# Optimization experiments

Measured on AMD Instinct MI355X. Metric: run time of the kernel, lower is better.

Reference implementation:

```python
import jax, jax.numpy as jnp
import numpy as np

EPS = 0.05
ITERS = 3


def setup_inputs() -> dict:
    key = jax.random.key(0)
    ks = jax.random.split(key, 20)
    B, C, H, W, TD = 2, 256, 64, 64, 512
    s = 0.02
    inp = {
        "img_feat": jax.random.normal(ks[0], (B, C, H, W), jnp.float32),
        "txt_feat": jax.random.normal(ks[1], (B, TD), jnp.float32),
        "density_map": jax.random.uniform(ks[2], (B, 1, H, W), jnp.float32),
        # text_proj
        "Wt": jax.random.normal(ks[3], (C, TD), jnp.float32) * s,
        "bt": jnp.zeros((C,), jnp.float32),
        # gamma_fc / beta_fc
        "Wg": jax.random.normal(ks[4], (C, C), jnp.float32) * s,
        "bg": jnp.zeros((C,), jnp.float32),
        "Wb": jax.random.normal(ks[5], (C, C), jnp.float32) * s,
        "bb": jnp.zeros((C,), jnp.float32),
        # out_proj 1x1 conv as [O, I]
        "Wo": jax.random.normal(ks[6], (C, C), jnp.float32) * s,
        "bo": jnp.zeros((C,), jnp.float32),
        # heatmap head: conv3x3 -> BN -> ReLU -> conv1x1
        "Wc1": jax.random.normal(ks[7], (C // 2, C, 3, 3), jnp.float32) * s,
        "bc1": jnp.zeros((C // 2,), jnp.float32),
        "bn_g": jnp.ones((C // 2,), jnp.float32),
        "bn_b": jnp.zeros((C // 2,), jnp.float32),
        "Wc2": jax.random.normal(ks[8], (2, C // 2), jnp.float32) * s,
        "bc2": jnp.zeros((2,), jnp.float32),
    }
    return inp


def reference(img_feat, txt_feat, density_map, Wt, bt, Wg, bg, Wb, bb,
              Wo, bo, Wc1, bc1, bn_g, bn_b, Wc2, bc2):
    B, C, H, W = img_feat.shape
    N = H * W

    # FiLM-style modulation from text
    txt_emb = txt_feat @ Wt.T + bt                         # [B, C]
    gamma = (txt_emb @ Wg.T + bg)[:, :, None, None]        # [B, C, 1, 1]
    beta = (txt_emb @ Wb.T + bb)[:, :, None, None]
    mod = img_feat * (1.0 + gamma) + beta                  # [B, C, H, W]

    source_feat = mod.reshape(B, C, N).transpose(0, 2, 1)  # [B, N, C]

    # marginals
    target = jax.nn.relu(density_map.reshape(B, N)) + 1e-6
    q = target / jnp.sum(target, axis=1, keepdims=True)    # [B, N]
    p = jnp.full((B, N), 1.0 / N, img_feat.dtype)

    # cosine-similarity cost and Gibbs kernel
    src_n = source_feat / jnp.maximum(
        jnp.linalg.norm(source_feat, axis=2, keepdims=True), 1e-12)
    sim = jnp.einsum('bnc,bmc->bnm', src_n, src_n)         # [B, N, N]
    K = jnp.exp(-(1.0 - sim) / EPS)

    # Sinkhorn iterations (fixed count)
    u = jnp.ones_like(p)
    v = jnp.ones_like(q)
    for _ in range(ITERS):
        v = q / (jnp.einsum('bnm,bn->bm', K, u) + 1e-8)
        u = p / (jnp.einsum('bnm,bm->bn', K, v) + 1e-8)

    T = u[:, :, None] * K * v[:, None, :]                  # transport plan
    fused = jnp.einsum('bnm,bnc->bmc', T, source_feat)     # T^T @ source
    fused = fused.transpose(0, 2, 1).reshape(B, C, H, W)

    out_feat = img_feat + jnp.einsum('oc,bchw->bohw', Wo, fused) + bo[None, :, None, None]

    # heatmap head
    h = jax.lax.conv_general_dilated(
        out_feat, Wc1, window_strides=(1, 1), padding='SAME',
        dimension_numbers=('NCHW', 'OIHW', 'NCHW')) + bc1[None, :, None, None]
    m = jnp.mean(h, axis=(0, 2, 3), keepdims=True)
    var = jnp.var(h, axis=(0, 2, 3), keepdims=True)
    h = (h - m) * jax.lax.rsqrt(var + 1e-5)
    h = jax.nn.relu(h * bn_g[None, :, None, None] + bn_b[None, :, None, None])
    heatmap = jnp.einsum('oc,bchw->bohw', Wc2, h) + bc2[None, :, None, None]

    return out_feat, heatmap
```

## Files before the change

### kernel.cpp

```cpp
#include <hip/hip_runtime.h>
#include <stdint.h>

#define B_   2
#define C_   256
#define N_   4096
#define TD_  512
#define OC_  128
#define PW_  66
#define PA_  4356

typedef float  f32x4  __attribute__((ext_vector_type(4)));
typedef short  bf16x8 __attribute__((ext_vector_type(8)));
typedef unsigned short u16;
typedef unsigned char  u8;

__device__ __forceinline__ u16 f2bf(float x){
  union { float f; uint32_t u; } v; v.f = x;
  uint32_t r = v.u + 0x7fffu + ((v.u >> 16) & 1u);
  return (u16)(r >> 16);
}
__device__ __forceinline__ uint32_t f2e5m2(float x){
  x = fminf(fmaxf(x, -57344.f), 57344.f);
  union { _Float16 h; u16 u; } c; c.h = (_Float16)x;
  uint32_t hb = c.u;
  return ((hb + 0x7fu + ((hb >> 8) & 1u)) >> 8) & 0xffu;
}
__device__ __forceinline__ float e5m2f(uint32_t byte){
  union { u16 u; _Float16 h; } c; c.u = (u16)(byte << 8);
  return (float)c.h;
}

__device__ __forceinline__ void gld_lds16(const void* g, void* l){
  __builtin_amdgcn_global_load_lds(
      (const __attribute__((address_space(1))) unsigned int*)g,
      (__attribute__((address_space(3))) unsigned int*)l,
      16, 0, 0);
}

__global__ __launch_bounds__(1024) void k_prep(
    const float* __restrict__ txt, const float* __restrict__ Wt, const float* __restrict__ bt,
    const float* __restrict__ Wg, const float* __restrict__ bg,
    const float* __restrict__ Wb, const float* __restrict__ bb,
    const float* __restrict__ dens, const float* __restrict__ Wo, const float* __restrict__ Wc1,
    float* __restrict__ gamma, float* __restrict__ beta,
    float* __restrict__ q, float* __restrict__ u,
    u16* __restrict__ Wo_bf, u16* __restrict__ Wc1r, u16* __restrict__ P){
  int bid = blockIdx.x;
  int t = threadIdx.x;
  if (bid < 2){
    int b = bid;
    __shared__ float ts[TD_];
    __shared__ float te[C_];
    if (t < TD_) ts[t] = txt[b*TD_ + t];
    __syncthreads();
    {
      int c = t >> 2, p = t & 3;
      const float4* w4 = (const float4*)(Wt + (size_t)c*TD_ + p*128);
      const float4* t4 = (const float4*)(ts + p*128);
      float a = 0.f;
      #pragma unroll 8
      for (int j = 0; j < 32; j++){
        float4 wv = w4[j], tv = t4[j];
        a += wv.x*tv.x + wv.y*tv.y + wv.z*tv.z + wv.w*tv.w;
      }
      a += __shfl_xor(a, 1);
      a += __shfl_xor(a, 2);
      if (p == 0) te[c] = a + bt[c];
    }
    __syncthreads();
    {
      int c = t >> 2, qb = (t >> 1) & 1, p = t & 1;
      const float* W = qb ? Wb : Wg;
      const float4* w4 = (const float4*)(W + (size_t)c*C_ + p*128);
      const float4* t4 = (const float4*)(te + p*128);
      float a = 0.f;
      #pragma unroll 8
      for (int j = 0; j < 32; j++){
        float4 wv = w4[j], tv = t4[j];
        a += wv.x*tv.x + wv.y*tv.y + wv.z*tv.z + wv.w*tv.w;
      }
      a += __shfl_xor(a, 1);
      if (p == 0){
        if (qb) beta[b*C_ + c]  = a + bb[c];
        else    gamma[b*C_ + c] = a + bg[c];
      }
    }
  } else if (bid < 4){
    int b = bid - 2;
    __shared__ float red[1024];
    float s = 0.f;
    for (int i = t; i < N_; i += 1024){ float v = fmaxf(dens[b*N_ + i], 0.f) + 1e-6f; s += v; }
    red[t] = s; __syncthreads();
    for (int o = 512; o; o >>= 1){ if (t < o) red[t] += red[t + o]; __syncthreads(); }
    float invs = 1.f / red[0];
    for (int i = t; i < N_; i += 1024){
      float v = fmaxf(dens[b*N_ + i], 0.f) + 1e-6f;
      q[b*N_ + i] = v*invs;
      u[b*N_ + i] = 1.f;
    }
  } else if (bid < 292){
    int i = (bid - 4)*1024 + t;
    if (i < C_*C_) Wo_bf[i] = f2bf(Wo[i]);
    if (i < 9*OC_*C_){
      int s = i / (OC_*C_); int rem = i - s*(OC_*C_);
      int oc = rem >> 8; int ic = rem & 255;
      Wc1r[i] = f2bf(Wc1[((size_t)(oc*C_ + ic))*9 + s]);
    }
  } else {
    int g = (bid - 292)*1024 + t;
    if (g < 16640){
      int px_i = g >> 5, seg = g & 31;
      int b = (px_i >= 260) ? 1 : 0;
      int i = px_i - b*260;
      int row, col;
      if (i < 66)      { row = 0;  col = i; }
      else if (i < 132){ row = 65; col = i - 66; }
      else { int i2 = i - 132; row = 1 + (i2 >> 1); col = (i2 & 1) ? 65 : 0; }
      uint4 z; z.x = 0; z.y = 0; z.z = 0; z.w = 0;
      *(uint4*)((char*)P + ((size_t)(b*PA_ + row*PW_ + col))*512 + seg*16) = z;
    }
  }
}

__global__ __launch_bounds__(256) void k_build(
    const float* __restrict__ img, const float* __restrict__ gamma, const float* __restrict__ beta,
    u16* __restrict__ Sn){
  int b = blockIdx.y; int n0 = blockIdx.x*64;
  __shared__ float tile[C_][65];
  __shared__ float pss[4][64];
  __shared__ float inv[64];
  int t = threadIdx.x;
  int x = t & 63, cb = t >> 6;
  float ss = 0.f;
  for (int k = 0; k < 64; k++){
    int c = cb*64 + k;
    float v = img[((size_t)(b*C_ + c))*N_ + n0 + x];
    v = v*(1.f + gamma[b*C_ + c]) + beta[b*C_ + c];
    tile[c][x] = v;
    ss += v*v;
  }
  pss[cb][x] = ss;
  __syncthreads();
  if (t < 64){
    float s = pss[0][t] + pss[1][t] + pss[2][t] + pss[3][t];
    float nrm = sqrtf(s);
    inv[t] = 1.f / fmaxf(nrm, 1e-12f);
  }
  __syncthreads();
  for (int i = 0; i < 64; i++){
    int idx = i*256 + t;
    int c = idx & 255, nl = idx >> 8;
    Sn[((size_t)(b*N_ + n0 + nl))*C_ + c] = f2bf(tile[c][nl]*inv[nl]);
  }
}

__global__ __launch_bounds__(256) void k_simK(const u16* __restrict__ Sn, u8* __restrict__ K8,
                                              u8* __restrict__ flags){
  int idx = blockIdx.x;
  int b = blockIdx.z;
  int nt = (int)((sqrtf(8.f*idx + 1.f) - 1.f)*0.5f);
  while ((nt+1)*(nt+2)/2 <= idx) nt++;
  while (nt*(nt+1)/2 > idx) nt--;
  int mt = idx - nt*(nt+1)/2;
  __shared__ char smem[32768];
  __shared__ int fred[4];
  int t = threadIdx.x; int w = t >> 6; int l = t & 63;
  int wm = w >> 1, wn = w & 1;
  f32x4 acc[4][4] = {};
  const char* Ab = (const char*)(Sn + ((size_t)(b*N_ + mt*128))*C_);
  const char* Bb = (const char*)(Sn + ((size_t)(b*N_ + nt*128))*C_);
  for (int step = 0; step < 4; step++){
    __syncthreads();
    for (int r = 0; r < 4; r++){
      int off = r*4096 + t*16;
      int row = off >> 7;
      int col = (off & 127) ^ ((row & 7) << 4);
      gld_lds16(Ab + (size_t)row*512 + step*128 + col, smem + off);
      gld_lds16(Bb + (size_t)row*512 + step*128 + col, smem + 16384 + off);
    }
    __syncthreads();
    for (int kk = 0; kk < 2; kk++){
      bf16x8 af[4], bfv[4];
      for (int i = 0; i < 4; i++){
        int ra = wm*64 + i*16 + (l & 15);
        af[i]  = *(const bf16x8*)(smem + ((ra*128 + kk*64 + (l>>4)*16) ^ ((ra & 7) << 4)));
        int rb = wn*64 + i*16 + (l & 15);
        bfv[i] = *(const bf16x8*)(smem + 16384 + ((rb*128 + kk*64 + (l>>4)*16) ^ ((rb & 7) << 4)));
      }
      for (int i = 0; i < 4; i++)
        for (int j = 0; j < 4; j++)
          acc[i][j] = __builtin_amdgcn_mfma_f32_16x16x32_bf16(af[i], bfv[j], acc[i][j], 0, 0, 0);
    }
  }
  float tmax = -1.f;
  for (int i = 0; i < 4; i++)
    for (int j = 0; j < 4; j++){
      f32x4 a = acc[i][j];
      tmax = fmaxf(tmax, fmaxf(fmaxf(a[0], a[1]), fmaxf(a[2], a[3])));
    }
  int nz = __any(tmax > 0.40f) ? 1 : 0;
  if (l == 0) fred[w] = nz;
  __syncthreads();
  int F = fred[0] | fred[1] | fred[2] | fred[3];
  if (t == 0){
    flags[b*1024 + nt*32 + mt] = (u8)F;
    if (mt != nt) flags[b*1024 + mt*32 + nt] = (u8)F;
  }
  size_t gb  = ((size_t)(b*N_ + nt*128))*N_ + mt*128;
  size_t gb2 = ((size_t)(b*N_ + mt*128))*N_ + nt*128;
  if (!F){
    uint4 z; z.x = 0; z.y = 0; z.z = 0; z.w = 0;
    for (int p = 0; p < 4; p++){
      int id2 = p*256 + t;
      int R = id2 >> 3, sl = id2 & 7;
      *(uint4*)(K8 + gb + (size_t)R*N_ + sl*16) = z;
      if (mt != nt) *(uint4*)(K8 + gb2 + (size_t)R*N_ + sl*16) = z;
    }
    return;
  }
  u8* tile = (u8*)smem;
  uint32_t wds[4][4];
  for (int i = 0; i < 4; i++)
    for (int j = 0; j < 4; j++){
      int R  = wn*64 + j*16 + (l & 15);
      int Cc = wm*64 + i*16 + ((l >> 4) << 2);
      uint32_t wd =  f2e5m2(__expf((acc[i][j][0] - 1.f)*20.f))
                  | (f2e5m2(__expf((acc[i][j][1] - 1.f)*20.f)) << 8)
                  | (f2e5m2(__expf((acc[i][j][2] - 1.f)*20.f)) << 16)
                  | (f2e5m2(__expf((acc[i][j][3] - 1.f)*20.f)) << 24);
      wds[i][j] = wd;
      *(uint32_t*)(tile + ((R*128 + Cc) ^ ((R & 7) << 4))) = wd;
    }
  __syncthreads();
  for (int p = 0; p < 4; p++){
    int id2 = p*256 + t;
    int R = id2 >> 3, sl = id2 & 7;
    uint4 vv = *(const uint4*)(tile + ((R*128 + sl*16) ^ ((R & 7) << 4)));
    *(uint4*)(K8 + gb + (size_t)R*N_ + sl*16) = vv;
  }
  if (mt != nt){
    __syncthreads();
    for (int i = 0; i < 4; i++)
      for (int j = 0; j < 4; j++){
        int m0 = wm*64 + i*16 + ((l >> 4) << 2);
        int n  = wn*64 + j*16 + (l & 15);
        uint32_t wd = wds[i][j];
        for (int r = 0; r < 4; r++){
          int R = m0 + r;
          tile[(R*128 + n) ^ ((R & 7) << 4)] = (u8)(wd >> (8*r));
        }
      }
    __syncthreads();
    for (int p = 0; p < 4; p++){
      int id2 = p*256 + t;
      int R = id2 >> 3, sl = id2 & 7;
      uint4 vv = *(const uint4*)(tile + ((R*128 + sl*16) ^ ((R & 7) << 4)));
      *(uint4*)(K8 + gb2 + (size_t)R*N_ + sl*16) = vv;
    }
  }
}

__global__ __launch_bounds__(256) void k_matvec(
    const u8* __restrict__ K8, const u8* __restrict__ flags, const float* __restrict__ x,
    const float* __restrict__ q, float* __restrict__ out, int use_q){
  int w = threadIdx.x >> 6, l = threadIdx.x & 63;
  int row = blockIdx.x*4 + w;
  int b = row >> 12;
  const u8* kp = K8 + (size_t)row*N_;
  const float* xp = x + (size_t)b*N_;
  const u8* fr = flags + b*1024 + ((row & 4095) >> 7)*32;
  float s = 0.f;
  for (int it = 0; it < 8; it++){
    uint32_t f4 = *(const uint32_t*)(fr + it*4);
    if (!f4) continue;
    int n0 = it*512 + l*8;
    uint2 kv = *(const uint2*)(kp + n0);
    float4 x0 = *(const float4*)(xp + n0);
    float4 x1 = *(const float4*)(xp + n0 + 4);
    s += e5m2f( kv.x        & 0xff)*x0.x + e5m2f((kv.x >>  8) & 0xff)*x0.y
       + e5m2f((kv.x >> 16) & 0xff)*x0.z + e5m2f( kv.x >> 24        )*x0.w;
    s += e5m2f( kv.y        & 0xff)*x1.x + e5m2f((kv.y >>  8) & 0xff)*x1.y
       + e5m2f((kv.y >> 16) & 0xff)*x1.z + e5m2f( kv.y >> 24        )*x1.w;
  }
  for (int o = 32; o; o >>= 1) s += __shfl_down(s, o);
  if (l == 0){
    float marg = use_q ? q[row] : 2.44140625e-4f;
    out[row] = marg / (s + 1e-8f);
  }
}

__global__ __launch_bounds__(256) void k_uS(
    const float* __restrict__ img, const float* __restrict__ gamma, const float* __restrict__ beta,
    const float* __restrict__ u, u8* __restrict__ uS8){
  size_t i = ((size_t)blockIdx.x*256 + threadIdx.x)*4;
  int n = (int)(i & (N_ - 1));
  size_t bc = i >> 12;
  int b = (int)(bc >> 8);
  float gm = 1.f + gamma[bc];
  float bt = beta[bc];
  float4 v  = *(const float4*)(img + i);
  float4 uu = *(const float4*)(u + (size_t)b*N_ + n);
  uint32_t o =  f2e5m2((v.x*gm + bt)*uu.x)
             | (f2e5m2((v.y*gm + bt)*uu.y) << 8)
             | (f2e5m2((v.z*gm + bt)*uu.z) << 16)
             | (f2e5m2((v.w*gm + bt)*uu.w) << 24);
  *(uint32_t*)(uS8 + i) = o;
}

__global__ __launch_bounds__(256) void k_fused_part(
    const u8* __restrict__ K8, const u8* __restrict__ uS8, const u8* __restrict__ flags,
    _Float16* __restrict__ part){
  int ct = blockIdx.x & 1, ks = blockIdx.x >> 1;
  int mt = blockIdx.y, b = blockIdx.z;
  __shared__ char smem[32768];
  int t = threadIdx.x, w = t >> 6, l = t & 63;
  int wc = w >> 1, wm = w & 1;
  f32x4 acc[4][4] = {};
  const u8* Ab = uS8 + ((size_t)(b*C_ + ct*128))*N_ + ks*1024;
  const u8* Bb = K8  + ((size_t)(b*N_ + mt*128))*N_ + ks*1024;
  const u8* fr = flags + b*1024 + mt*32 + ks*8;
  for (int step = 0; step < 8; step++){
    if (!fr[step]) continue;
    __syncthreads();
    for (int r = 0; r < 4; r++){
      int off = r*4096 + t*16;
      int row = off >> 7;
      int col = (off & 127) ^ ((row & 7) << 4);
      gld_lds16(Ab + (size_t)row*N_ + step*128 + col, smem + off);
      gld_lds16(Bb + (size_t)row*N_ + step*128 + col, smem + 16384 + off);
    }
    __syncthreads();
    for (int kk = 0; kk < 4; kk++){
      long av[4], bv[4];
      for (int i = 0; i < 4; i++){
        int ra = wc*64 + i*16 + (l & 15);
        av[i] = *(const long*)(smem + ((ra*128 + kk*32 + (l>>4)*8) ^ ((ra & 7) << 4)));
        int rb = wm*64 + i*16 + (l & 15);
        bv[i] = *(const long*)(smem + 16384 + ((rb*128 + kk*32 + (l>>4)*8) ^ ((rb & 7) << 4)));
      }
      for (int i = 0; i < 4; i++)
        for (int j = 0; j < 4; j++)
          acc[i][j] = __builtin_amdgcn_mfma_f32_16x16x32_bf8_bf8(av[i], bv[j], acc[i][j], 0, 0, 0);
    }
  }
  _Float16* pp = part + ((size_t)(ks*2 + b))*N_*C_;
  for (int i = 0; i < 4; i++)
    for (int j = 0; j < 4; j++){
      int c0 = ct*128 + wc*64 + i*16 + ((l >> 4) << 2);
      int m  = mt*128 + wm*64 + j*16 + (l & 15);
      union { _Float16 h[4]; ushort4 u; } pk;
      pk.h[0] = (_Float16)acc[i][j][0];
      pk.h[1] = (_Float16)acc[i][j][1];
      pk.h[2] = (_Float16)acc[i][j][2];
      pk.h[3] = (_Float16)acc[i][j][3];
      *(ushort4*)(pp + (size_t)m*C_ + c0) = pk.u;
    }
}

__global__ __launch_bounds__(256) void k_reduce(
    const _Float16* __restrict__ part, const float* __restrict__ vvec, u16* __restrict__ fused){
  int idx = blockIdx.x*256 + threadIdx.x;
  int c0 = (idx & 63) * 4;
  int bm = idx >> 6;
  float vm = vvec[bm];
  float s0 = 0.f, s1 = 0.f, s2 = 0.f, s3 = 0.f;
  int b = bm >> 12, m = bm & 4095;
  for (int sp = 0; sp < 4; sp++){
    union { ushort4 u; _Float16 h[4]; } pk;
    pk.u = *(const ushort4*)(part + (((size_t)(sp*2 + b))*N_ + m)*C_ + c0);
    s0 += (float)pk.h[0]; s1 += (float)pk.h[1];
    s2 += (float)pk.h[2]; s3 += (float)pk.h[3];
  }
  ushort4 o;
  o.x = f2bf(s0*vm); o.y = f2bf(s1*vm);
  o.z = f2bf(s2*vm); o.w = f2bf(s3*vm);
  *(ushort4*)(fused + (size_t)bm*C_ + c0) = o;
}

__global__ __launch_bounds__(256) void k_outproj(
    const u16* __restrict__ fused, const u16* __restrict__ Wo_bf,
    const float* __restrict__ img, const float* __restrict__ bo,
    float* __restrict__ out, u16* __restrict__ P){
  int nt = blockIdx.x, ot = blockIdx.y, b = blockIdx.z;
  int t = threadIdx.x, w = t >> 6, l = t & 63;
  int wm = w >> 1, wn = w & 1;
  __shared__ u16 tile[128][72];
  f32x4 acc[4][2] = {};
  for (int kc = 0; kc < 8; kc++){
    bf16x8 af[4], bfv[2];
    for (int i = 0; i < 4; i++){
      int n = nt*128 + wm*64 + i*16 + (l & 15);
      af[i] = *(const bf16x8*)(fused + ((size_t)(b*N_ + n))*C_ + kc*32 + (l >> 4)*8);
    }
    for (int j = 0; j < 2; j++){
      int o = ot*64 + wn*32 + j*16 + (l & 15);
      bfv[j] = *(const bf16x8*)(Wo_bf + (size_t)o*C_ + kc*32 + (l >> 4)*8);
    }
    for (int i = 0; i < 4; i++)
      for (int j = 0; j < 2; j++)
        acc[i][j] = __builtin_amdgcn_mfma_f32_16x16x32_bf16(af[i], bfv[j], acc[i][j], 0, 0, 0);
  }
  for (int i = 0; i < 4; i++)
    for (int j = 0; j < 2; j++){
      int ol = wn*32 + j*16 + (l & 15);
      int o = ot*64 + ol;
      int nl = wm*64 + i*16 + ((l >> 4) << 2);
      int n = nt*128 + nl;
      size_t a = ((size_t)(b*C_ + o))*N_ + n;
      float4 iv = *(const float4*)(img + a);
      float bov = bo[o];
      float4 r;
      r.x = iv.x + acc[i][j][0] + bov;
      r.y = iv.y + acc[i][j][1] + bov;
      r.z = iv.z + acc[i][j][2] + bov;
      r.w = iv.w + acc[i][j][3] + bov;
      *(float4*)(out + a) = r;
      tile[nl+0][ol] = f2bf(r.x);
      tile[nl+1][ol] = f2bf(r.y);
      tile[nl+2][ol] = f2bf(r.z);
      tile[nl+3][ol] = f2bf(r.w);
    }
  __syncthreads();
  for (int p = 0; p < 4; p++){
    int idx = p*256 + t;
    int row = idx >> 3, seg = idx & 7;
    int n = nt*128 + row;
    int y = n >> 6, x = n & 63;
    uint4 vv = *(const uint4*)(&tile[row][seg*8]);
    *(uint4*)(P + ((size_t)(b*PA_ + (y+1)*PW_ + (x+1)))*C_ + ot*64 + seg*8) = vv;
  }
}

__global__ __launch_bounds__(256) void k_conv(
    const u16* __restrict__ P, const u16* __restrict__ Wc1r, float* __restrict__ convP){
  int pt = blockIdx.x;
  int sp = blockIdx.y;
  int b  = blockIdx.z;
  int dy = sp - 1;
  __shared__ char smem[32768];
  int t = threadIdx.x, w = t >> 6, l = t & 63;
  int wm = w >> 1, wn = w & 1;
  f32x4 acc[4][4] = {};
  int y0 = pt*2;
  size_t prow[4], wrow[4];
  int colsw[4];
  #pragma unroll
  for (int rr = 0; rr < 4; rr++){
    int off = rr*4096 + t*16;
    int row = off >> 7;
    int col = (off & 127) ^ ((row & 7) << 4);
    colsw[rr] = col;
    int gy = row >> 6, gx = row & 63;
    prow[rr] = ((size_t)(b*PA_ + (y0 + gy + dy + 1)*PW_ + gx + 1))*512;
    wrow[rr] = ((size_t)(sp*3*128 + row))*512;
  }
  const char* Pb = (const char*)P;
  const char* Wb = (const char*)Wc1r;
  for (int step = 0; step < 12; step++){
    int dxi = step >> 2, c64 = step & 3;
    __syncthreads();
    #pragma unroll
    for (int rr = 0; rr < 4; rr++){
      int off = rr*4096 + t*16;
      gld_lds16(Wb + wrow[rr] + (size_t)dxi*65536 + c64*128 + colsw[rr], smem + off);
      gld_lds16(Pb + prow[rr] + (dxi-1)*512 + c64*128 + colsw[rr], smem + 16384 + off);
    }
    __syncthreads();
    for (int kk = 0; kk < 2; kk++){
      bf16x8 af[4], bv[4];
      for (int i = 0; i < 4; i++){
        int ra = wm*64 + i*16 + (l & 15);
        af[i] = *(const bf16x8*)(smem + ((ra*128 + kk*64 + (l>>4)*16) ^ ((ra & 7) << 4)));
        int rb = wn*64 + i*16 + (l & 15);
        bv[i] = *(const bf16x8*)(smem + 16384 + ((rb*128 + kk*64 + (l>>4)*16) ^ ((rb & 7) << 4)));
      }
      for (int i = 0; i < 4; i++)
        for (int j = 0; j < 4; j++)
          acc[i][j] = __builtin_amdgcn_mfma_f32_16x16x32_bf16(af[i], bv[j], acc[i][j], 0, 0, 0);
    }
  }
  float* pp = convP + (((size_t)(sp*2 + b))*N_ + (size_t)pt*128)*OC_;
  for (int i = 0; i < 4; i++)
    for (int j = 0; j < 4; j++){
      int pxl = wn*64 + j*16 + (l & 15);
      int ocl = wm*64 + i*16 + ((l >> 4) << 2);
      float4 r; r.x = acc[i][j][0]; r.y = acc[i][j][1]; r.z = acc[i][j][2]; r.w = acc[i][j][3];
      *(float4*)(pp + (size_t)pxl*OC_ + ocl) = r;
    }
}

__global__ __launch_bounds__(256) void k_stats(
    const float* __restrict__ convP, const float* __restrict__ bc1,
    float* __restrict__ h, float* __restrict__ pSum, float* __restrict__ pSsq){
  int blk = blockIdx.x;
  int t = threadIdx.x; int c = t & 127, half = t >> 7;
  __shared__ float s1[256], s2[256];
  float bias = bc1[c];
  float a = 0.f, b2 = 0.f;
  int R0 = blk*128 + half*64;
  for (int r = 0; r < 64; r++){
    size_t base = (size_t)(R0 + r)*OC_ + c;
    float v = convP[base] + convP[base + (size_t)8192*OC_] + convP[base + (size_t)16384*OC_] + bias;
    h[base] = v;
    a += v; b2 += v*v;
  }
  s1[t] = a; s2[t] = b2;
  __syncthreads();
  if (t < 128){
    pSum[blk*128 + c] = s1[t] + s1[t + 128];
    pSsq[blk*128 + c] = s2[t] + s2[t + 128];
  }
}

__global__ __launch_bounds__(256) void k_head(
    const float* __restrict__ h, const float* __restrict__ pSum, const float* __restrict__ pSsq,
    const float* __restrict__ bn_g, const float* __restrict__ bn_b,
    const float* __restrict__ Wc2, const float* __restrict__ bc2, float* __restrict__ hm){
  __shared__ float sc[128], sh[128], w0[128], w1[128];
  __shared__ float rs[256], rss[256];
  int t = threadIdx.x;
  {
    int c = t & 127, half = t >> 7;
    float s = 0.f, ss = 0.f;
    for (int k = half*32; k < half*32 + 32; k++){
      s += pSum[k*128 + c]; ss += pSsq[k*128 + c];
    }
    rs[t] = s; rss[t] = ss;
  }
  __syncthreads();
  if (t < 128){
    float s = rs[t] + rs[t+128], ss = rss[t] + rss[t+128];
    float m = s*(1.f/8192.f);
    float var = ss*(1.f/8192.f) - m*m;
    float scv = bn_g[t]*rsqrtf(var + 1e-5f);
    sc[t] = scv; sh[t] = bn_b[t] - m*scv;
    w0[t] = Wc2[t]; w1[t] = Wc2[128 + t];
  }
  __syncthreads();
  int n = blockIdx.x*256 + t;
  const float* hp = h + (size_t)n*OC_;
  float a0 = bc2[0], a1 = bc2[1];
  for (int c4 = 0; c4 < 32; c4++){
    float4 hv = *(const float4*)(hp + c4*4);
    int c = c4*4;
    float r;
    r = fmaxf(hv.x*sc[c]   + sh[c],   0.f); a0 += w0[c]*r;   a1 += w1[c]*r;
    r = fmaxf(hv.y*sc[c+1] + sh[c+1], 0.f); a0 += w0[c+1]*r; a1 += w1[c+1]*r;
    r = fmaxf(hv.z*sc[c+2] + sh[c+2], 0.f); a0 += w0[c+2]*r; a1 += w1[c+2]*r;
    r = fmaxf(hv.w*sc[c+3] + sh[c+3], 0.f); a0 += w0[c+3]*r; a1 += w1[c+3]*r;
  }
  int b = n >> 12, p = n & 4095;
  hm[((size_t)(b*2 + 0))*N_ + p] = a0;
  hm[((size_t)(b*2 + 1))*N_ + p] = a1;
}

extern "C" void kernel_launch(void* const* d_in, const int* in_sizes, int n_in,
                              void* d_out, int out_size, void* d_ws, size_t ws_size,
                              hipStream_t stream){
  const float* img  = (const float*)d_in[0];
  const float* txt  = (const float*)d_in[1];
  const float* dens = (const float*)d_in[2];
  const float* Wt   = (const float*)d_in[3];
  const float* bt   = (const float*)d_in[4];
  const float* Wg   = (const float*)d_in[5];
  const float* bg   = (const float*)d_in[6];
  const float* Wb   = (const float*)d_in[7];
  const float* bb   = (const float*)d_in[8];
  const float* Wo   = (const float*)d_in[9];
  const float* bo   = (const float*)d_in[10];
  const float* Wc1  = (const float*)d_in[11];
  const float* bc1  = (const float*)d_in[12];
  const float* bng  = (const float*)d_in[13];
  const float* bnb  = (const float*)d_in[14];
  const float* Wc2  = (const float*)d_in[15];
  const float* bc2  = (const float*)d_in[16];

  char* ws = (char*)d_ws;
  u8*       K8     = (u8*)      (ws + 0);
  u16*      Sn     = (u16*)     (ws + 33554432);
  u8*       uS8    = (u8*)      (ws + 37748736);
  _Float16* partH  = (_Float16*)(ws + 39845888);
  u16*      fused  = (u16*)     (ws + 56623104);
  u16*      P      = (u16*)     (ws + 60817408);
  float*    hbuf   = (float*)   (ws + 65277952);
  float*    convP  = (float*)   (ws + 69472256);
  float*    gamma  = (float*)   (ws + 82055168);
  float*    beta   = (float*)   (ws + 82057216);
  float*    q      = (float*)   (ws + 82059264);
  float*    u      = (float*)   (ws + 82092032);
  float*    v      = (float*)   (ws + 82124800);
  u16*      Wo_bf  = (u16*)     (ws + 82157568);
  u16*      Wc1r   = (u16*)     (ws + 82288640);
  float*    pSum   = (float*)   (ws + 82878464);
  float*    pSsq   = (float*)   (ws + 82911232);
  u8*       flags  = (u8*)      (ws + 82944000);

  float* outp = (float*)d_out;
  float* hm   = outp + 2*C_*N_;

  k_prep  <<<309, 1024, 0, stream>>>(txt, Wt, bt, Wg, bg, Wb, bb, dens, Wo, Wc1,
                                     gamma, beta, q, u, Wo_bf, Wc1r, P);
  k_build <<<dim3(64,2), 256, 0, stream>>>(img, gamma, beta, Sn);
  k_simK  <<<dim3(528,1,2), 256, 0, stream>>>(Sn, K8, flags);
  for (int it = 0; it < 3; it++){
    k_matvec<<<2048, 256, 0, stream>>>(K8, flags, u, q, v, 1);
    k_matvec<<<2048, 256, 0, stream>>>(K8, flags, v, q, u, 0);
  }
  k_uS        <<<2048, 256, 0, stream>>>(img, gamma, beta, u, uS8);
  k_fused_part<<<dim3(8,32,2), 256, 0, stream>>>(K8, uS8, flags, partH);
  k_reduce    <<<2048, 256, 0, stream>>>(partH, v, fused);
  k_outproj   <<<dim3(32,4,2), 256, 0, stream>>>(fused, Wo_bf, img, bo, outp, P);
  k_conv      <<<dim3(32,3,2), 256, 0, stream>>>(P, Wc1r, convP);
  k_stats     <<<64, 256, 0, stream>>>(convP, bc1, hbuf, pSum, pSsq);
  k_head      <<<32, 256, 0, stream>>>(hbuf, pSum, pSsq, bng, bnb, Wc2, bc2, hm);
}
```

Measured before the change: 155.1 us.

## Run Sinkhorn per connected block component in one kernel; drop split-K reduce

A single k_sink kernel builds the connectivity of nonzero K tiles from the flag map, finds the connected component containing each 128-row tile, and runs all six Sinkhorn mat-vec passes for that component inside one workgroup using shared memory. It then writes the u-scaled e5m2 source directly. This replaces the six k_matvec launches and the k_uS launch. The transport GEMM also drops its split-K partial buffer and separate reduce kernel, applying v and the bf16 conversion in its epilogue. The risk is that a large or dense component would be processed serially by one workgroup, and the GEMM now launches fewer blocks.

```diff
diff --git a/kernel.cpp b/kernel.cpp
--- a/kernel.cpp
+++ b/kernel.cpp
@@ -260,66 +260,108 @@
   }
 }
 
-__global__ __launch_bounds__(256) void k_matvec(
-    const u8* __restrict__ K8, const u8* __restrict__ flags, const float* __restrict__ x,
-    const float* __restrict__ q, float* __restrict__ out, int use_q){
-  int w = threadIdx.x >> 6, l = threadIdx.x & 63;
-  int row = blockIdx.x*4 + w;
-  int b = row >> 12;
-  const u8* kp = K8 + (size_t)row*N_;
-  const float* xp = x + (size_t)b*N_;
-  const u8* fr = flags + b*1024 + ((row & 4095) >> 7)*32;
-  float s = 0.f;
-  for (int it = 0; it < 8; it++){
-    uint32_t f4 = *(const uint32_t*)(fr + it*4);
-    if (!f4) continue;
-    int n0 = it*512 + l*8;
-    uint2 kv = *(const uint2*)(kp + n0);
-    float4 x0 = *(const float4*)(xp + n0);
-    float4 x1 = *(const float4*)(xp + n0 + 4);
-    s += e5m2f( kv.x        & 0xff)*x0.x + e5m2f((kv.x >>  8) & 0xff)*x0.y
-       + e5m2f((kv.x >> 16) & 0xff)*x0.z + e5m2f( kv.x >> 24        )*x0.w;
-    s += e5m2f( kv.y        & 0xff)*x1.x + e5m2f((kv.y >>  8) & 0xff)*x1.y
-       + e5m2f((kv.y >> 16) & 0xff)*x1.z + e5m2f( kv.y >> 24        )*x1.w;
-  }
-  for (int o = 32; o; o >>= 1) s += __shfl_down(s, o);
-  if (l == 0){
-    float marg = use_q ? q[row] : 2.44140625e-4f;
-    out[row] = marg / (s + 1e-8f);
-  }
-}
-
-__global__ __launch_bounds__(256) void k_uS(
-    const float* __restrict__ img, const float* __restrict__ gamma, const float* __restrict__ beta,
-    const float* __restrict__ u, u8* __restrict__ uS8){
-  size_t i = ((size_t)blockIdx.x*256 + threadIdx.x)*4;
-  int n = (int)(i & (N_ - 1));
-  size_t bc = i >> 12;
-  int b = (int)(bc >> 8);
-  float gm = 1.f + gamma[bc];
-  float bt = beta[bc];
-  float4 v  = *(const float4*)(img + i);
-  float4 uu = *(const float4*)(u + (size_t)b*N_ + n);
-  uint32_t o =  f2e5m2((v.x*gm + bt)*uu.x)
-             | (f2e5m2((v.y*gm + bt)*uu.y) << 8)
-             | (f2e5m2((v.z*gm + bt)*uu.z) << 16)
-             | (f2e5m2((v.w*gm + bt)*uu.w) << 24);
-  *(uint32_t*)(uS8 + i) = o;
-}
-
-__global__ __launch_bounds__(256) void k_fused_part(
+__global__ __launch_bounds__(256) void k_sink(
+    const u8* __restrict__ K8, const u8* __restrict__ flags,
+    const float* __restrict__ q,
+    const float* __restrict__ img, const float* __restrict__ gamma,
+    const float* __restrict__ beta,
+    float* __restrict__ u, float* __restrict__ v, u8* __restrict__ uS8){
+  int r = blockIdx.x, b = blockIdx.y;
+  int t = threadIdx.x;
+  __shared__ uint32_t mask[32];
+  __shared__ uint32_t comp_s;
+  __shared__ u8 tl[32];
+  __shared__ int scnt;
+  __shared__ float xb[4096];
+  __shared__ float yb[4096];
+  if (t < 32){
+    const u8* fr = flags + b*1024 + t*32;
+    uint32_t m = 0;
+    for (int j = 0; j < 32; j++) m |= (uint32_t)(fr[j] != 0) << j;
+    mask[t] = m;
+  }
+  __syncthreads();
+  if (t == 0){
+    uint32_t comp = 1u << r;
+    for (int it = 0; it < 32; it++){
+      uint32_t nc = comp;
+      for (int i = 0; i < 32; i++) if ((comp >> i) & 1u) nc |= mask[i];
+      if (nc == comp) break;
+      comp = nc;
+    }
+    comp_s = comp;
+    int c = 0;
+    for (int i = 0; i < 32; i++) if ((comp >> i) & 1u) tl[c++] = (u8)i;
+    scnt = c;
+  }
+  __syncthreads();
+  uint32_t comp = comp_s;
+  if (comp & ((1u << r) - 1u)) return;
+  int s = scnt;
+  int R = s*128;
+  for (int i = t; i < R; i += 256) xb[i] = 1.f;
+  __syncthreads();
+  for (int it = 0; it < 6; it++){
+    int use_q = !(it & 1);
+    for (int ri = t; ri < R; ri += 256){
+      int gm = tl[ri >> 7]*128 + (ri & 127);
+      const u8* kp = K8 + ((size_t)(b*N_ + gm))*N_;
+      float ssum = 0.f;
+      for (int ci = 0; ci < s; ci++){
+        const u8* kt = kp + tl[ci]*128;
+        const float* xp = xb + ci*128;
+        for (int kk = 0; kk < 16; kk++){
+          uint2 kv = *(const uint2*)(kt + kk*8);
+          const float* x8 = xp + kk*8;
+          ssum += e5m2f( kv.x        & 0xff)*x8[0] + e5m2f((kv.x >>  8) & 0xff)*x8[1]
+                + e5m2f((kv.x >> 16) & 0xff)*x8[2] + e5m2f( kv.x >> 24        )*x8[3];
+          ssum += e5m2f( kv.y        & 0xff)*x8[4] + e5m2f((kv.y >>  8) & 0xff)*x8[5]
+                + e5m2f((kv.y >> 16) & 0xff)*x8[6] + e5m2f( kv.y >> 24        )*x8[7];
+        }
+      }
+      float marg = use_q ? q[b*N_ + gm] : 2.44140625e-4f;
+      yb[ri] = marg / (ssum + 1e-8f);
+    }
+    __syncthreads();
+    if (it == 4)
+      for (int i = t; i < R; i += 256) v[b*N_ + tl[i >> 7]*128 + (i & 127)] = yb[i];
+    if (it == 5)
+      for (int i = t; i < R; i += 256) u[b*N_ + tl[i >> 7]*128 + (i & 127)] = yb[i];
+    for (int i = t; i < R; i += 256) xb[i] = yb[i];
+    __syncthreads();
+  }
+  int qpc = R >> 2;
+  int quads = C_ * qpc;
+  for (int qd = t; qd < quads; qd += 256){
+    int c  = qd / qpc;
+    int nq = qd - c*qpc;
+    int ri = nq*4;
+    int n = tl[ri >> 7]*128 + (ri & 127);
+    size_t bc = (size_t)(b*C_ + c);
+    float gm = 1.f + gamma[bc];
+    float bt = beta[bc];
+    float4 vi = *(const float4*)(img + bc*N_ + n);
+    uint32_t o =  f2e5m2((vi.x*gm + bt)*xb[ri+0])
+               | (f2e5m2((vi.y*gm + bt)*xb[ri+1]) << 8)
+               | (f2e5m2((vi.z*gm + bt)*xb[ri+2]) << 16)
+               | (f2e5m2((vi.w*gm + bt)*xb[ri+3]) << 24);
+    *(uint32_t*)(uS8 + bc*N_ + n) = o;
+  }
+}
+
+__global__ __launch_bounds__(256) void k_fused(
     const u8* __restrict__ K8, const u8* __restrict__ uS8, const u8* __restrict__ flags,
-    _Float16* __restrict__ part){
-  int ct = blockIdx.x & 1, ks = blockIdx.x >> 1;
+    const float* __restrict__ vvec, u16* __restrict__ fused){
+  int ct = blockIdx.x;
   int mt = blockIdx.y, b = blockIdx.z;
   __shared__ char smem[32768];
   int t = threadIdx.x, w = t >> 6, l = t & 63;
   int wc = w >> 1, wm = w & 1;
   f32x4 acc[4][4] = {};
-  const u8* Ab = uS8 + ((size_t)(b*C_ + ct*128))*N_ + ks*1024;
-  const u8* Bb = K8  + ((size_t)(b*N_ + mt*128))*N_ + ks*1024;
-  const u8* fr = flags + b*1024 + mt*32 + ks*8;
-  for (int step = 0; step < 8; step++){
+  const u8* Ab = uS8 + ((size_t)(b*C_ + ct*128))*N_;
+  const u8* Bb = K8  + ((size_t)(b*N_ + mt*128))*N_;
+  const u8* fr = flags + b*1024 + mt*32;
+  for (int step = 0; step < 32; step++){
     if (!fr[step]) continue;
     __syncthreads();
     for (int r = 0; r < 4; r++){
@@ -343,38 +385,19 @@
           acc[i][j] = __builtin_amdgcn_mfma_f32_16x16x32_bf8_bf8(av[i], bv[j], acc[i][j], 0, 0, 0);
     }
   }
-  _Float16* pp = part + ((size_t)(ks*2 + b))*N_*C_;
-  for (int i = 0; i < 4; i++)
-    for (int j = 0; j < 4; j++){
+  for (int j = 0; j < 4; j++){
+    int m = mt*128 + wm*64 + j*16 + (l & 15);
+    float vm = vvec[b*N_ + m];
+    for (int i = 0; i < 4; i++){
       int c0 = ct*128 + wc*64 + i*16 + ((l >> 4) << 2);
-      int m  = mt*128 + wm*64 + j*16 + (l & 15);
-      union { _Float16 h[4]; ushort4 u; } pk;
-      pk.h[0] = (_Float16)acc[i][j][0];
-      pk.h[1] = (_Float16)acc[i][j][1];
-      pk.h[2] = (_Float16)acc[i][j][2];
-      pk.h[3] = (_Float16)acc[i][j][3];
-      *(ushort4*)(pp + (size_t)m*C_ + c0) = pk.u;
-    }
-}
-
-__global__ __launch_bounds__(256) void k_reduce(
-    const _Float16* __restrict__ part, const float* __restrict__ vvec, u16* __restrict__ fused){
-  int idx = blockIdx.x*256 + threadIdx.x;
-  int c0 = (idx & 63) * 4;
-  int bm = idx >> 6;
-  float vm = vvec[bm];
-  float s0 = 0.f, s1 = 0.f, s2 = 0.f, s3 = 0.f;
-  int b = bm >> 12, m = bm & 4095;
-  for (int sp = 0; sp < 4; sp++){
-    union { ushort4 u; _Float16 h[4]; } pk;
-    pk.u = *(const ushort4*)(part + (((size_t)(sp*2 + b))*N_ + m)*C_ + c0);
-    s0 += (float)pk.h[0]; s1 += (float)pk.h[1];
-    s2 += (float)pk.h[2]; s3 += (float)pk.h[3];
-  }
-  ushort4 o;
-  o.x = f2bf(s0*vm); o.y = f2bf(s1*vm);
-  o.z = f2bf(s2*vm); o.w = f2bf(s3*vm);
-  *(ushort4*)(fused + (size_t)bm*C_ + c0) = o;
+      ushort4 o;
+      o.x = f2bf(acc[i][j][0]*vm);
+      o.y = f2bf(acc[i][j][1]*vm);
+      o.z = f2bf(acc[i][j][2]*vm);
+      o.w = f2bf(acc[i][j][3]*vm);
+      *(ushort4*)(fused + ((size_t)(b*N_ + m))*C_ + c0) = o;
+    }
+  }
 }
 
 __global__ __launch_bounds__(256) void k_outproj(
@@ -579,7 +602,6 @@
   u8*       K8     = (u8*)      (ws + 0);
   u16*      Sn     = (u16*)     (ws + 33554432);
   u8*       uS8    = (u8*)      (ws + 37748736);
-  _Float16* partH  = (_Float16*)(ws + 39845888);
   u16*      fused  = (u16*)     (ws + 56623104);
   u16*      P      = (u16*)     (ws + 60817408);
   float*    hbuf   = (float*)   (ws + 65277952);
@@ -602,15 +624,10 @@
                                      gamma, beta, q, u, Wo_bf, Wc1r, P);
   k_build <<<dim3(64,2), 256, 0, stream>>>(img, gamma, beta, Sn);
   k_simK  <<<dim3(528,1,2), 256, 0, stream>>>(Sn, K8, flags);
-  for (int it = 0; it < 3; it++){
-    k_matvec<<<2048, 256, 0, stream>>>(K8, flags, u, q, v, 1);
-    k_matvec<<<2048, 256, 0, stream>>>(K8, flags, v, q, u, 0);
-  }
-  k_uS        <<<2048, 256, 0, stream>>>(img, gamma, beta, u, uS8);
-  k_fused_part<<<dim3(8,32,2), 256, 0, stream>>>(K8, uS8, flags, partH);
-  k_reduce    <<<2048, 256, 0, stream>>>(partH, v, fused);
-  k_outproj   <<<dim3(32,4,2), 256, 0, stream>>>(fused, Wo_bf, img, bo, outp, P);
-  k_conv      <<<dim3(32,3,2), 256, 0, stream>>>(P, Wc1r, convP);
-  k_stats     <<<64, 256, 0, stream>>>(convP, bc1, hbuf, pSum, pSsq);
-  k_head      <<<32, 256, 0, stream>>>(hbuf, pSum, pSsq, bng, bnb, Wc2, bc2, hm);
-}
+  k_sink  <<<dim3(32,2), 256, 0, stream>>>(K8, flags, q, img, gamma, beta, u, v, uS8);
+  k_fused <<<dim3(2,32,2), 256, 0, stream>>>(K8, uS8, flags, v, fused);
+  k_outproj<<<dim3(32,4,2), 256, 0, stream>>>(fused, Wo_bf, img, bo, outp, P);
+  k_conv  <<<dim3(32,3,2), 256, 0, stream>>>(P, Wc1r, convP);
+  k_stats <<<64, 256, 0, stream>>>(convP, bc1, hbuf, pSum, pSsq);
+  k_head  <<<32, 256, 0, stream>>>(hbuf, pSum, pSsq, bng, bnb, Wc2, bc2, hm);
+}
```

After: 142.7 us. 1.09x faster.
